# Kernel tuning notes

Hardware: AMD Instinct MI355X
Metric: run time of the kernel (lower is better)

The kernel has to match this reference:

```python
import jax, jax.numpy as jnp
import numpy as np

BATCH = 1024
M = 64      # N_v measurements
N = 8192    # N_theta unknowns
STEPS = 3   # N_admm_steps
EPS_DIV = 1e-12


def setup_inputs() -> dict:
    key = jax.random.key(0)
    k = jax.random.split(key, 4)
    return {
        "r_n": jax.random.normal(k[0], (BATCH, 2, N), jnp.float32),
        "y": jax.random.normal(k[1], (BATCH, 2, M), jnp.float32),
        "u_in": jax.random.normal(k[2], (BATCH, 2, M), jnp.float32),
        "A": jax.random.normal(k[3], (2, M, N), jnp.float32) / np.sqrt(N).astype(np.float32),
        "log_rho": jnp.zeros((), jnp.float32),                 # rho = 1.0
        "log_epsilon": jnp.asarray(np.log(0.01), jnp.float32), # epsilon = 0.01
    }


def _cmm(Ar, Ai, v):
    # complex matmul A @ v : v [b,2,N] -> [b,2,M]
    vr, vi = v[:, 0], v[:, 1]
    return jnp.stack([vr @ Ar.T - vi @ Ai.T, vi @ Ar.T + vr @ Ai.T], axis=1)


def _chm(Ar, Ai, v):
    # complex conj-transpose matmul A^H @ v : v [b,2,M] -> [b,2,N]
    vr, vi = v[:, 0], v[:, 1]
    return jnp.stack([vr @ Ar + vi @ Ai, vi @ Ar - vr @ Ai], axis=1)


def reference(r_n, y, u_in, A, log_rho, log_epsilon):
    rho = jnp.exp(log_rho)
    epsilon = jnp.exp(log_epsilon)
    Ar, Ai = A[0], A[1]  # [M, N]

    # SMW system matrix: S = (1/rho) I + A A^H, written as real 2Mx2M block matrix.
    # It is constant across ADMM steps (rho fixed within a forward pass).
    I_M = jnp.eye(M, dtype=A.dtype)
    S_r = I_M / (rho + EPS_DIV) + Ar @ Ar.T + Ai @ Ai.T
    S_i = Ai @ Ar.T - Ar @ Ai.T
    S_block = jnp.block([[S_r, -S_i], [S_i, S_r]])  # [2M, 2M]

    x, z, u = r_n, y, u_in
    for _ in range(STEPS):
        # x-update via SMW: x = b - A^H (S^{-1} A b), b = r_n + rho A^H (z - u)
        b = r_n + rho * _chm(Ar, Ai, z - u)          # [b,2,N]
        Ab = _cmm(Ar, Ai, b)                          # [b,2,M]
        R = jnp.concatenate([Ab[:, 0], Ab[:, 1]], axis=1)  # [b,2M]
        sol = jnp.linalg.solve(S_block, R.T)          # [2M, b]
        T = jnp.stack([sol[:M].T, sol[M:].T], axis=1)  # [b,2,M]
        x = b - _chm(Ar, Ai, T)                       # [b,2,N]
        # enforce_real: zero imaginary part; enforce_positivity: clamp real part
        x = jnp.stack([jnp.maximum(x[:, 0], 0.0), jnp.zeros_like(x[:, 0])], axis=1)
        # z-update: project residual onto complex L2 ball of radius epsilon
        Ax = _cmm(Ar, Ai, x)                          # [b,2,M]
        v = Ax + u - y
        nrm = jnp.sqrt(jnp.sum(v * v, axis=(1, 2), keepdims=True))
        z = y + v * jnp.minimum(1.0, epsilon / (nrm + EPS_DIV))
        # dual update
        u = u + Ax - z
    return x, u
```

## Files before the change

kernel.cpp:

```cpp
#include <hip/hip_runtime.h>

#define B_ 1024
#define M_ 64
#define N_ 8192
#define NSG 16
#define NS3 8

typedef __attribute__((ext_vector_type(8))) short bf16x8;
typedef __attribute__((ext_vector_type(4))) float f32x4;

__device__ inline unsigned short f2b(float f) {
    union { float f; unsigned u; } v; v.f = f;
    unsigned r = v.u + 0x7FFFu + ((v.u >> 16) & 1u);
    return (unsigned short)(r >> 16);
}
__device__ inline unsigned rne2(float lo, float hi) {
    union { float f; unsigned u; } a, b; a.f = lo; b.f = hi;
    unsigned x = (a.u + 0x7FFFu + ((a.u >> 16) & 1u)) >> 16;
    unsigned y = (b.u + 0x7FFFu + ((b.u >> 16) & 1u)) >> 16;
    return x | (y << 16);
}
__device__ inline float b2f(unsigned short s) {
    union { unsigned u; float f; } v; v.u = ((unsigned)s) << 16; return v.f;
}
__device__ inline float rl(float v, int l) {
    return __builtin_bit_cast(float, __builtin_amdgcn_readlane(__builtin_bit_cast(int, v), l));
}

__global__ __launch_bounds__(256) void k_cvt(const float* src, unsigned short* dst) {
    size_t i = ((size_t)blockIdx.x * 256 + threadIdx.x) * 8;
    float4 f0 = *(const float4*)(src + i);
    float4 f1 = *(const float4*)(src + i + 4);
    union { bf16x8 v; unsigned u[4]; } r;
    r.u[0] = rne2(f0.x, f0.y); r.u[1] = rne2(f0.z, f0.w);
    r.u[2] = rne2(f1.x, f1.y); r.u[3] = rne2(f1.z, f1.w);
    *(bf16x8*)(dst + i) = r.v;
}

__global__ __launch_bounds__(256) void k_prep(const float* A, unsigned short* Abf,
                                              unsigned short* WgT, unsigned short* ATb,
                                              float* out) {
    if (blockIdx.x >= 128) {
        int z = blockIdx.x - 128;
        int fi = z * 4096 + threadIdx.x * 16;
        int b = fi >> 13;
        int n = fi & 8191;
        float4* p = (float4*)(out + (size_t)b * 16384 + 8192 + n);
        float4 z4 = make_float4(0.f, 0.f, 0.f, 0.f);
        p[0] = z4; p[1] = z4; p[2] = z4; p[3] = z4;
        return;
    }
    __shared__ float tile[128][65];
    int n0 = blockIdx.x * 64;
    int t = threadIdx.x;
    int nl = t % 64, r0 = t / 64;
#pragma unroll
    for (int it = 0; it < 32; ++it) {
        int row = r0 + it * 4;
        tile[row][nl] = A[(size_t)row * N_ + n0 + nl];
    }
    __syncthreads();
#pragma unroll
    for (int it = 0; it < 32; ++it) {
        int row = r0 + it * 4;
        float v = tile[row][nl];
        unsigned short bv = f2b(v);
        Abf[(size_t)row * N_ + n0 + nl] = bv;
        if (row < 64) {
            WgT[(size_t)row * 16384 + n0 + nl] = bv;
            WgT[(size_t)(64 + row) * 16384 + 8192 + n0 + nl] = bv;
        } else {
            int m = row - 64;
            WgT[(size_t)m * 16384 + 8192 + n0 + nl] = f2b(-v);
            WgT[(size_t)(64 + m) * 16384 + n0 + nl] = bv;
        }
    }
    int o = t % 128, nn0 = t / 128;
#pragma unroll
    for (int it = 0; it < 32; ++it) {
        int nn = nn0 + it * 2;
        ATb[(size_t)(n0 + nn) * 128 + o] = f2b(tile[o][nn]);
    }
}

__global__ __launch_bounds__(256) void k_Sbuild(const float* A, const float* lr,
                                                float* S, float* AAHT) {
    __shared__ float redS[8];
    int bid = blockIdx.x;
    int i = 0, rem = bid;
    while (rem >= 64 - i) { rem -= 64 - i; ++i; }
    int j = i + rem;
    int t = threadIdx.x;
    const float* Ar = A;
    const float* Ai = A + (size_t)M_ * N_;
    const float* ari = Ar + (size_t)i * N_;
    const float* aii = Ai + (size_t)i * N_;
    const float* arj = Ar + (size_t)j * N_;
    const float* aij = Ai + (size_t)j * N_;
    float aR = 0.f, aI = 0.f;
#pragma unroll
    for (int it = 0; it < 8; ++it) {
        int n = it * 1024 + t * 4;
        float4 xr = *(const float4*)(ari + n);
        float4 xi = *(const float4*)(aii + n);
        float4 br = *(const float4*)(arj + n);
        float4 bi = *(const float4*)(aij + n);
        aR += xr.x * br.x + xi.x * bi.x + xr.y * br.y + xi.y * bi.y
            + xr.z * br.z + xi.z * bi.z + xr.w * br.w + xi.w * bi.w;
        aI += xi.x * br.x - xr.x * bi.x + xi.y * br.y - xr.y * bi.y
            + xi.z * br.z - xr.z * bi.z + xi.w * br.w - xr.w * bi.w;
    }
    for (int off = 32; off > 0; off >>= 1) {
        aR += __shfl_down(aR, off, 64);
        aI += __shfl_down(aI, off, 64);
    }
    int lane = t & 63, w = t >> 6;
    if (lane == 0) { redS[w * 2] = aR; redS[w * 2 + 1] = aI; }
    __syncthreads();
    if (t == 0) {
        float R = redS[0] + redS[2] + redS[4] + redS[6];
        float I = redS[1] + redS[3] + redS[5] + redS[7];
        float inv_rho = 1.0f / (expf(lr[0]) + 1e-12f);
        float diag = (i == j) ? inv_rho : 0.f;
        S[((size_t)i * 64 + j) * 2 + 0] = R + diag;
        S[((size_t)i * 64 + j) * 2 + 1] = I;
        AAHT[((size_t)j * 64 + i) * 2 + 0] = R;
        AAHT[((size_t)j * 64 + i) * 2 + 1] = I;
        if (i != j) {
            S[((size_t)j * 64 + i) * 2 + 0] = R;
            S[((size_t)j * 64 + i) * 2 + 1] = -I;
            AAHT[((size_t)i * 64 + j) * 2 + 0] = R;
            AAHT[((size_t)i * 64 + j) * 2 + 1] = -I;
        }
    }
}

__global__ __launch_bounds__(256, 2) void k_Ginv(const unsigned short* rnb,
                                                 const unsigned short* WgT,
                                                 float* Gpart,
                                                 const float* S, float* Wt) {
    int t = threadIdx.x;
    int lane = t & 63;
    if (blockIdx.x == 0) {
        __builtin_amdgcn_s_setprio(1);
        __shared__ float2 Tp[2][4][64];
        int g = t >> 6;
        float mx0,my0,mx1,my1,mx2,my2,mx3,my3,mx4,my4,mx5,my5,mx6,my6,mx7,my7;
        float mx8,my8,mx9,my9,mx10,my10,mx11,my11,mx12,my12,mx13,my13,mx14,my14,mx15,my15;
#define GJ_INIT(J) { int c = 16 * ((J) >> 2) + 4 * g + ((J) & 3);            \
    float2 v = ((const float2*)S)[(size_t)lane * 64 + c];                    \
    mx##J = v.x; my##J = v.y; }
        GJ_INIT(0) GJ_INIT(1) GJ_INIT(2) GJ_INIT(3) GJ_INIT(4) GJ_INIT(5) GJ_INIT(6) GJ_INIT(7)
        GJ_INIT(8) GJ_INIT(9) GJ_INIT(10) GJ_INIT(11) GJ_INIT(12) GJ_INIT(13) GJ_INIT(14) GJ_INIT(15)
#undef GJ_INIT

#define PIV(JA, JB0, JB1, JB2, jj) {                                         \
    int k = p4 + (jj);                                                       \
    float px = rl(mx##JA, k), py = rl(my##JA, k);                            \
    float d = px * px + py * py;                                             \
    float id = 1.0f / d;                                                     \
    float pix = px * id, piy = -py * id;                                     \
    bool isk = (lane == k);                                                  \
    float a   = isk ? 0.f : 1.f;                                             \
    float fpx = isk ? -pix : (mx##JA * pix - my##JA * piy);                  \
    float fpy = isk ? -piy : (mx##JA * piy + my##JA * pix);                  \
    { float sx = rl(mx##JB0, k), sy = rl(my##JB0, k);                        \
      float nx = a * mx##JB0 - (fpx * sx - fpy * sy);                        \
      float ny = a * my##JB0 - (fpx * sy + fpy * sx);                        \
      mx##JB0 = nx; my##JB0 = ny; }                                          \
    { float sx = rl(mx##JB1, k), sy = rl(my##JB1, k);                        \
      float nx = a * mx##JB1 - (fpx * sx - fpy * sy);                        \
      float ny = a * my##JB1 - (fpx * sy + fpy * sx);                        \
      mx##JB1 = nx; my##JB1 = ny; }                                          \
    { float sx = rl(mx##JB2, k), sy = rl(my##JB2, k);                        \
      float nx = a * mx##JB2 - (fpx * sx - fpy * sy);                        \
      float ny = a * my##JB2 - (fpx * sy + fpy * sx);                        \
      mx##JB2 = nx; my##JB2 = ny; }                                          \
    mx##JA = -fpx; my##JA = -fpy; }

#define FACT4(J0, J1, J2, J3) {                                              \
    PIV(J0, J1, J2, J3, 0) PIV(J1, J0, J2, J3, 1)                            \
    PIV(J2, J0, J1, J3, 2) PIV(J3, J0, J1, J2, 3)                            \
    Tp[buf][0][lane] = make_float2(mx##J0, my##J0);                          \
    Tp[buf][1][lane] = make_float2(mx##J1, my##J1);                          \
    Tp[buf][2][lane] = make_float2(mx##J2, my##J2);                          \
    Tp[buf][3][lane] = make_float2(mx##J3, my##J3); }

        for (int p = 0; p < 16; ++p) {
            const int buf = p & 1;
            const int p4  = p * 4;
            const int q   = p >> 2;
            const bool own = (g == (p & 3));
            if (own) {
                switch (q) {
                    case 0:  FACT4(0, 1, 2, 3)     break;
                    case 1:  FACT4(4, 5, 6, 7)     break;
                    case 2:  FACT4(8, 9, 10, 11)   break;
                    default: FACT4(12, 13, 14, 15) break;
                }
            }
            __syncthreads();
            float2 t0 = Tp[buf][0][lane];
            float2 t1 = Tp[buf][1][lane];
            float2 t2 = Tp[buf][2][lane];
            float2 t3 = Tp[buf][3][lane];
            float msk = ((lane >> 2) == p) ? 0.f : 1.f;
            int skipq = own ? q : -1;
#define TRAIL(J) if (((J) >> 2) != skipq) {                                  \
    float s0x = rl(mx##J, p4),     s0y = rl(my##J, p4);                      \
    float s1x = rl(mx##J, p4 + 1), s1y = rl(my##J, p4 + 1);                  \
    float s2x = rl(mx##J, p4 + 2), s2y = rl(my##J, p4 + 2);                  \
    float s3x = rl(mx##J, p4 + 3), s3y = rl(my##J, p4 + 3);                  \
    float ax = msk * mx##J, ay = msk * my##J;                                \
    ax += t0.x * s0x - t0.y * s0y; ay += t0.x * s0y + t0.y * s0x;            \
    ax += t1.x * s1x - t1.y * s1y; ay += t1.x * s1y + t1.y * s1x;            \
    ax += t2.x * s2x - t2.y * s2y; ay += t2.x * s2y + t2.y * s2x;            \
    ax += t3.x * s3x - t3.y * s3y; ay += t3.x * s3y + t3.y * s3x;            \
    mx##J = ax; my##J = ay; }
            TRAIL(0)  TRAIL(1)  TRAIL(2)  TRAIL(3)
            TRAIL(4)  TRAIL(5)  TRAIL(6)  TRAIL(7)
            TRAIL(8)  TRAIL(9)  TRAIL(10) TRAIL(11)
            TRAIL(12) TRAIL(13) TRAIL(14) TRAIL(15)
#undef TRAIL
        }
#undef FACT4
#undef PIV
#define GJ_OUT(J) { int c = 16 * ((J) >> 2) + 4 * g + ((J) & 3);             \
    ((float2*)Wt)[(size_t)c * 64 + lane] = make_float2(mx##J, my##J); }
        GJ_OUT(0) GJ_OUT(1) GJ_OUT(2) GJ_OUT(3) GJ_OUT(4) GJ_OUT(5) GJ_OUT(6) GJ_OUT(7)
        GJ_OUT(8) GJ_OUT(9) GJ_OUT(10) GJ_OUT(11) GJ_OUT(12) GJ_OUT(13) GJ_OUT(14) GJ_OUT(15)
#undef GJ_OUT
        __builtin_amdgcn_s_setprio(0);
    }
    int bx = blockIdx.x;
    int w = t >> 6;
    int l15 = lane & 15;
    int q8 = (lane >> 4) * 8;
    int split = bx & 15;
    int b0 = (bx >> 4) * 32;
    int k0 = split * 1024;
    f32x4 a00 = {}, a01 = {}, a10 = {}, a11 = {};
    const unsigned short* x0 = rnb + (size_t)(b0 + l15) * 16384 + k0 + q8;
    const unsigned short* x1 = x0 + (size_t)16 * 16384;
    const unsigned short* w0 = WgT + (size_t)(w * 32 + l15) * 16384 + k0 + q8;
    const unsigned short* w1 = w0 + (size_t)16 * 16384;
#pragma unroll 8
    for (int ks = 0; ks < 32; ++ks) {
        int kk = ks * 32;
        bf16x8 af0 = *(const bf16x8*)(x0 + kk);
        bf16x8 af1 = *(const bf16x8*)(x1 + kk);
        bf16x8 bf0 = *(const bf16x8*)(w0 + kk);
        bf16x8 bf1 = *(const bf16x8*)(w1 + kk);
        a00 = __builtin_amdgcn_mfma_f32_16x16x32_bf16(af0, bf0, a00, 0, 0, 0);
        a01 = __builtin_amdgcn_mfma_f32_16x16x32_bf16(af0, bf1, a01, 0, 0, 0);
        a10 = __builtin_amdgcn_mfma_f32_16x16x32_bf16(af1, bf0, a10, 0, 0, 0);
        a11 = __builtin_amdgcn_mfma_f32_16x16x32_bf16(af1, bf1, a11, 0, 0, 0);
    }
    int row = (lane >> 4) * 4;
    size_t base = (size_t)split * (B_ * 128);
    float* g  = Gpart + base + (size_t)(b0 + row) * 128 + w * 32 + l15;
    float* g2 = g + 16 * 128;
#pragma unroll
    for (int r = 0; r < 4; ++r) {
        g[(size_t)r * 128]       = a00[r];
        g[(size_t)r * 128 + 16]  = a01[r];
        g2[(size_t)r * 128]      = a10[r];
        g2[(size_t)r * 128 + 16] = a11[r];
    }
}

__global__ __launch_bounds__(256) void k_F(const float* Gpart, const float* AAHT,
                                           const float* Wt, const float* Axpart,
                                           const float* y, const float* uprev,
                                           float* u, const float* lr, const float* le,
                                           unsigned short* qb, int have_ax) {
    __shared__ float wS[128];
    __shared__ float2 partA[4][64];
    __shared__ float2 partB[4][64];
    __shared__ float2 AbS[64];
    __shared__ float red[2];
    int t = threadIdx.x;
    int b = blockIdx.x;
    float rho = expf(lr[0]);
    if (have_ax) {
        float vv = 0.f, uo = 0.f, yv = 0.f, ax = 0.f;
        if (t < 128) {
            size_t idx = (size_t)b * 128 + t;
            #pragma unroll
            for (int s = 0; s < NS3; ++s) ax += Axpart[(size_t)s * 131072 + idx];
            uo = uprev[idx]; yv = y[idx];
            vv = ax + uo - yv;
            float sq = vv * vv;
            for (int off = 32; off > 0; off >>= 1) sq += __shfl_down(sq, off, 64);
            if ((t & 63) == 0) red[t >> 6] = sq;
        }
        __syncthreads();
        if (t < 128) {
            float tot = red[0] + red[1];
            float eps = expf(le[0]);
            float scale = fminf(1.f, eps / (sqrtf(tot) + 1e-12f));
            float zv = yv + vv * scale;
            float un = uo + ax - zv;
            u[(size_t)b * 128 + t] = un;
            wS[t] = zv - un;
        }
    } else {
        if (t < 128) {
            size_t idx = (size_t)b * 128 + t;
            wS[t] = y[idx] - uprev[idx];
        }
    }
    __syncthreads();
    int m = t & 63;
    int w = __builtin_amdgcn_readfirstlane(t >> 6);
    float aR = 0.f, aI = 0.f;
#pragma unroll
    for (int kk = 0; kk < 16; ++kk) {
        int k = w * 16 + kk;
        float wr = wS[k];
        float wi = wS[64 + k];
        float2 h = *(const float2*)(AAHT + ((size_t)k * 64 + m) * 2);
        aR += wr * h.x - wi * h.y;
        aI += wi * h.x + wr * h.y;
    }
    aR *= rho; aI *= rho;
#pragma unroll
    for (int s4 = 0; s4 < 4; ++s4) {
        int s = w * 4 + s4;
        aR += Gpart[(size_t)s * 131072 + (size_t)b * 128 + m];
        aI += Gpart[(size_t)s * 131072 + (size_t)b * 128 + 64 + m];
    }
    partA[w][m] = make_float2(aR, aI);
    __syncthreads();
    if (w == 0) {
        float2 p0 = partA[0][m], p1 = partA[1][m], p2 = partA[2][m], p3 = partA[3][m];
        AbS[m] = make_float2(p0.x + p1.x + p2.x + p3.x, p0.y + p1.y + p2.y + p3.y);
    }
    __syncthreads();
    float tR = 0.f, tI = 0.f;
#pragma unroll
    for (int kk = 0; kk < 16; ++kk) {
        int k = w * 16 + kk;
        float2 Wv = *(const float2*)(Wt + ((size_t)k * 64 + m) * 2);
        float2 ab = AbS[k];
        tR += ab.x * Wv.x - ab.y * Wv.y;
        tI += ab.y * Wv.x + ab.x * Wv.y;
    }
    partB[w][m] = make_float2(tR, tI);
    __syncthreads();
    if (w == 0) {
        float2 q0 = partB[0][m], q1 = partB[1][m], q2 = partB[2][m], q3 = partB[3][m];
        float sR = q0.x + q1.x + q2.x + q3.x;
        float sI = q0.y + q1.y + q2.y + q3.y;
        qb[(size_t)b * 128 + m] = f2b(rho * wS[m] - sR);
        qb[(size_t)b * 128 + 64 + m] = f2b(rho * wS[64 + m] - sI);
    }
}

__global__ __launch_bounds__(512, 2) void k_H23(const unsigned short* qb, const unsigned short* ATb,
                                                const unsigned short* rnb, const unsigned short* Abf,
                                                float* out, float* Axpart, int last) {
    __shared__ __align__(16) char lds_buf[8 * 8448];
    int t = threadIdx.x;
    int lane = t & 63;
    int w = t >> 6;
    int l15 = lane & 15;
    int q8 = (lane >> 4) * 8;
    int row = (lane >> 4) * 4;
    int slab = blockIdx.x;
    int b0 = blockIdx.y * 16;
    int n0 = slab * 1024 + w * 128;
    short* xs = (short*)(lds_buf + w * 8448);
    float* rs = (float*)(lds_buf + w * 8448);

    bf16x8 a[4];
    const unsigned short* qrow = qb + (size_t)(b0 + l15) * 128 + q8;
#pragma unroll
    for (int ks = 0; ks < 4; ++ks) a[ks] = *(const bf16x8*)(qrow + ks * 32);
#pragma unroll 2
    for (int nt = 0; nt < 8; ++nt) {
        f32x4 acc = {};
        const unsigned short* bbase = ATb + (size_t)(n0 + nt * 16 + l15) * 128 + q8;
#pragma unroll
        for (int ks = 0; ks < 4; ++ks) {
            bf16x8 bf = *(const bf16x8*)(bbase + ks * 32);
            acc = __builtin_amdgcn_mfma_f32_16x16x32_bf16(a[ks], bf, acc, 0, 0, 0);
        }
        int ncol = n0 + nt * 16 + l15;
        int nloc = nt * 16 + l15;
#pragma unroll
        for (int r = 0; r < 4; ++r) {
            size_t ridx = (size_t)(b0 + row + r) * 16384 + ncol;
            float v = fmaxf(acc[r] + b2f(rnb[ridx]), 0.f);
            if (last) out[ridx] = v;
            xs[(row + r) * 264 + nloc] = (short)f2b(v);
        }
    }
    f32x4 acc8[8] = {};
#pragma unroll
    for (int ks = 0; ks < 4; ++ks) {
        bf16x8 xf = *(const bf16x8*)(xs + l15 * 264 + ks * 32 + q8);
#pragma unroll
        for (int ot = 0; ot < 8; ++ot) {
            const unsigned short* bp = Abf + (size_t)(ot * 16 + l15) * 8192 + n0 + ks * 32 + q8;
            acc8[ot] = __builtin_amdgcn_mfma_f32_16x16x32_bf16(xf, *(const bf16x8*)bp, acc8[ot], 0, 0, 0);
        }
    }
    __syncthreads();
#pragma unroll
    for (int ot = 0; ot < 8; ++ot)
#pragma unroll
        for (int r = 0; r < 4; ++r)
            rs[(row + r) * 132 + ot * 16 + l15] = acc8[ot][r];
    __syncthreads();
#pragma unroll
    for (int e = t; e < 2048; e += 512) {
        int b = e >> 7, o = e & 127;
        float sAx = 0.f;
#pragma unroll
        for (int ww = 0; ww < 8; ++ww)
            sAx += ((const float*)(lds_buf + ww * 8448))[b * 132 + o];
        Axpart[(size_t)slab * 131072 + (size_t)(b0 + b) * 128 + o] = sAx;
    }
}

__global__ __launch_bounds__(128) void k_small3f(const float* Axpart, const float* uprev,
                                                 const float* y, const float* le,
                                                 float* uout) {
    __shared__ float red[2];
    int b = blockIdx.x, t = threadIdx.x;
    size_t idx = (size_t)b * 128 + t;
    float ax = 0.f;
#pragma unroll
    for (int s = 0; s < NS3; ++s) ax += Axpart[(size_t)s * 131072 + idx];
    float uo = uprev[idx], yv = y[idx];
    float v = ax + uo - yv;
    float sq = v * v;
    for (int off = 32; off > 0; off >>= 1) sq += __shfl_down(sq, off, 64);
    if ((t & 63) == 0) red[t >> 6] = sq;
    __syncthreads();
    float tot = red[0] + red[1];
    float eps = expf(le[0]);
    float scale = fminf(1.f, eps / (sqrtf(tot) + 1e-12f));
    float zv = yv + v * scale;
    float un = uo + ax - zv;
    uout[idx] = un;
}

extern "C" void kernel_launch(void* const* d_in, const int* in_sizes, int n_in,
                              void* d_out, int out_size, void* d_ws, size_t ws_size,
                              hipStream_t stream) {
    const float* rn  = (const float*)d_in[0];
    const float* y   = (const float*)d_in[1];
    const float* uin = (const float*)d_in[2];
    const float* A   = (const float*)d_in[3];
    const float* lr  = (const float*)d_in[4];
    const float* le  = (const float*)d_in[5];

    float* out = (float*)d_out;
    float* ws  = (float*)d_ws;

    float* Gpart  = ws;
    float* Axpart = Gpart + (size_t)NSG * 131072;
    float* S      = Axpart + (size_t)NS3 * 131072;
    float* AAHT   = S + 8192;
    float* Wt     = AAHT + 8192;
    float* z      = Wt + 8192;
    float* u      = z + 131072;
    unsigned short* qb  = (unsigned short*)(u + 131072);
    unsigned short* rnb = qb + 131072;
    unsigned short* WgT = rnb + (size_t)B_ * 16384;
    unsigned short* Abf = WgT + 2097152;
    unsigned short* ATb = Abf + 1048576;
    float* uout = out + (size_t)B_ * 2 * N_;

    k_prep<<<2176, 256, 0, stream>>>(A, Abf, WgT, ATb, out);
    k_cvt<<<8192, 256, 0, stream>>>(rn, rnb);
    k_Sbuild<<<2080, 256, 0, stream>>>(A, lr, S, AAHT);
    k_Ginv<<<512, 256, 0, stream>>>(rnb, WgT, Gpart, S, Wt);

    k_F<<<B_, 256, 0, stream>>>(Gpart, AAHT, Wt, Axpart, y, uin, u, lr, le, qb, 0);
    k_H23<<<dim3(NS3, 64), 512, 0, stream>>>(qb, ATb, rnb, Abf, out, Axpart, 0);
    k_F<<<B_, 256, 0, stream>>>(Gpart, AAHT, Wt, Axpart, y, uin, u, lr, le, qb, 1);
    k_H23<<<dim3(NS3, 64), 512, 0, stream>>>(qb, ATb, rnb, Abf, out, Axpart, 0);
    k_F<<<B_, 256, 0, stream>>>(Gpart, AAHT, Wt, Axpart, y, u, u, lr, le, qb, 1);
    k_H23<<<dim3(NS3, 64), 512, 0, stream>>>(qb, ATb, rnb, Abf, out, Axpart, 1);
    k_small3f<<<B_, 128, 0, stream>>>(Axpart, u, y, le, uout);
}
```

Measured before the change: 337.9 us.

## Split Gauss-Jordan into own kernel, halve H23 slab width, broadcast pivot rows via LDS

Moves the 64x64 complex Gauss-Jordan inversion out of block 0 of k_Ginv into a separate single-block kernel. It also replaces the per-column readlane pivot-row broadcasts with an LDS staging buffer (Srow). k_H23 now covers 512 columns per slab across 16 slabs instead of 1024 across 8, which shrinks LDS use and adds a two-phase in-LDS reduction of the per-wave partial results. The intent is more parallelism and occupancy in the x/Ax kernel and shorter serial chains in GJ. In exchange, k_small3f reads more Axpart partials, the GJ step becomes a serial one-block launch, and an unused z buffer is dropped from the workspace.

```diff
diff --git a/kernel.cpp b/kernel.cpp
--- a/kernel.cpp
+++ b/kernel.cpp
@@ -4,7 +4,7 @@
 #define M_ 64
 #define N_ 8192
 #define NSG 16
-#define NS3 8
+#define NS3 16
 
 typedef __attribute__((ext_vector_type(8))) short bf16x8;
 typedef __attribute__((ext_vector_type(4))) float f32x4;
@@ -135,23 +135,19 @@
     }
 }
 
-__global__ __launch_bounds__(256, 2) void k_Ginv(const unsigned short* rnb,
-                                                 const unsigned short* WgT,
-                                                 float* Gpart,
-                                                 const float* S, float* Wt) {
+__global__ __launch_bounds__(256) void k_gj(const float* S, float* Wt) {
     int t = threadIdx.x;
     int lane = t & 63;
-    if (blockIdx.x == 0) {
-        __builtin_amdgcn_s_setprio(1);
-        __shared__ float2 Tp[2][4][64];
-        int g = t >> 6;
-        float mx0,my0,mx1,my1,mx2,my2,mx3,my3,mx4,my4,mx5,my5,mx6,my6,mx7,my7;
-        float mx8,my8,mx9,my9,mx10,my10,mx11,my11,mx12,my12,mx13,my13,mx14,my14,mx15,my15;
+    int g = t >> 6;
+    __shared__ float2 Tp[2][4][64];
+    __shared__ float2 Srow[4][4][16];
+    float mx0,my0,mx1,my1,mx2,my2,mx3,my3,mx4,my4,mx5,my5,mx6,my6,mx7,my7;
+    float mx8,my8,mx9,my9,mx10,my10,mx11,my11,mx12,my12,mx13,my13,mx14,my14,mx15,my15;
 #define GJ_INIT(J) { int c = 16 * ((J) >> 2) + 4 * g + ((J) & 3);            \
     float2 v = ((const float2*)S)[(size_t)lane * 64 + c];                    \
     mx##J = v.x; my##J = v.y; }
-        GJ_INIT(0) GJ_INIT(1) GJ_INIT(2) GJ_INIT(3) GJ_INIT(4) GJ_INIT(5) GJ_INIT(6) GJ_INIT(7)
-        GJ_INIT(8) GJ_INIT(9) GJ_INIT(10) GJ_INIT(11) GJ_INIT(12) GJ_INIT(13) GJ_INIT(14) GJ_INIT(15)
+    GJ_INIT(0) GJ_INIT(1) GJ_INIT(2) GJ_INIT(3) GJ_INIT(4) GJ_INIT(5) GJ_INIT(6) GJ_INIT(7)
+    GJ_INIT(8) GJ_INIT(9) GJ_INIT(10) GJ_INIT(11) GJ_INIT(12) GJ_INIT(13) GJ_INIT(14) GJ_INIT(15)
 #undef GJ_INIT
 
 #define PIV(JA, JB0, JB1, JB2, jj) {                                         \
@@ -186,52 +182,74 @@
     Tp[buf][2][lane] = make_float2(mx##J2, my##J2);                          \
     Tp[buf][3][lane] = make_float2(mx##J3, my##J3); }
 
-        for (int p = 0; p < 16; ++p) {
-            const int buf = p & 1;
-            const int p4  = p * 4;
-            const int q   = p >> 2;
-            const bool own = (g == (p & 3));
-            if (own) {
-                switch (q) {
-                    case 0:  FACT4(0, 1, 2, 3)     break;
-                    case 1:  FACT4(4, 5, 6, 7)     break;
-                    case 2:  FACT4(8, 9, 10, 11)   break;
-                    default: FACT4(12, 13, 14, 15) break;
-                }
+    for (int p = 0; p < 16; ++p) {
+        const int buf = p & 1;
+        const int p4  = p * 4;
+        const int q   = p >> 2;
+        const bool own = (g == (p & 3));
+        if ((lane >> 2) == p) {
+            int j = lane & 3;
+            Srow[g][j][0]  = make_float2(mx0,  my0);
+            Srow[g][j][1]  = make_float2(mx1,  my1);
+            Srow[g][j][2]  = make_float2(mx2,  my2);
+            Srow[g][j][3]  = make_float2(mx3,  my3);
+            Srow[g][j][4]  = make_float2(mx4,  my4);
+            Srow[g][j][5]  = make_float2(mx5,  my5);
+            Srow[g][j][6]  = make_float2(mx6,  my6);
+            Srow[g][j][7]  = make_float2(mx7,  my7);
+            Srow[g][j][8]  = make_float2(mx8,  my8);
+            Srow[g][j][9]  = make_float2(mx9,  my9);
+            Srow[g][j][10] = make_float2(mx10, my10);
+            Srow[g][j][11] = make_float2(mx11, my11);
+            Srow[g][j][12] = make_float2(mx12, my12);
+            Srow[g][j][13] = make_float2(mx13, my13);
+            Srow[g][j][14] = make_float2(mx14, my14);
+            Srow[g][j][15] = make_float2(mx15, my15);
+        }
+        if (own) {
+            switch (q) {
+                case 0:  FACT4(0, 1, 2, 3)     break;
+                case 1:  FACT4(4, 5, 6, 7)     break;
+                case 2:  FACT4(8, 9, 10, 11)   break;
+                default: FACT4(12, 13, 14, 15) break;
             }
-            __syncthreads();
-            float2 t0 = Tp[buf][0][lane];
-            float2 t1 = Tp[buf][1][lane];
-            float2 t2 = Tp[buf][2][lane];
-            float2 t3 = Tp[buf][3][lane];
-            float msk = ((lane >> 2) == p) ? 0.f : 1.f;
-            int skipq = own ? q : -1;
+        }
+        __syncthreads();
+        float2 t0 = Tp[buf][0][lane];
+        float2 t1 = Tp[buf][1][lane];
+        float2 t2 = Tp[buf][2][lane];
+        float2 t3 = Tp[buf][3][lane];
+        float msk = ((lane >> 2) == p) ? 0.f : 1.f;
+        int skipq = own ? q : -1;
 #define TRAIL(J) if (((J) >> 2) != skipq) {                                  \
-    float s0x = rl(mx##J, p4),     s0y = rl(my##J, p4);                      \
-    float s1x = rl(mx##J, p4 + 1), s1y = rl(my##J, p4 + 1);                  \
-    float s2x = rl(mx##J, p4 + 2), s2y = rl(my##J, p4 + 2);                  \
-    float s3x = rl(mx##J, p4 + 3), s3y = rl(my##J, p4 + 3);                  \
+    float2 s0 = Srow[g][0][J], s1 = Srow[g][1][J];                           \
+    float2 s2 = Srow[g][2][J], s3 = Srow[g][3][J];                           \
     float ax = msk * mx##J, ay = msk * my##J;                                \
-    ax += t0.x * s0x - t0.y * s0y; ay += t0.x * s0y + t0.y * s0x;            \
-    ax += t1.x * s1x - t1.y * s1y; ay += t1.x * s1y + t1.y * s1x;            \
-    ax += t2.x * s2x - t2.y * s2y; ay += t2.x * s2y + t2.y * s2x;            \
-    ax += t3.x * s3x - t3.y * s3y; ay += t3.x * s3y + t3.y * s3x;            \
+    ax += t0.x * s0.x - t0.y * s0.y; ay += t0.x * s0.y + t0.y * s0.x;        \
+    ax += t1.x * s1.x - t1.y * s1.y; ay += t1.x * s1.y + t1.y * s1.x;        \
+    ax += t2.x * s2.x - t2.y * s2.y; ay += t2.x * s2.y + t2.y * s2.x;        \
+    ax += t3.x * s3.x - t3.y * s3.y; ay += t3.x * s3.y + t3.y * s3.x;        \
     mx##J = ax; my##J = ay; }
-            TRAIL(0)  TRAIL(1)  TRAIL(2)  TRAIL(3)
-            TRAIL(4)  TRAIL(5)  TRAIL(6)  TRAIL(7)
-            TRAIL(8)  TRAIL(9)  TRAIL(10) TRAIL(11)
-            TRAIL(12) TRAIL(13) TRAIL(14) TRAIL(15)
+        TRAIL(0)  TRAIL(1)  TRAIL(2)  TRAIL(3)
+        TRAIL(4)  TRAIL(5)  TRAIL(6)  TRAIL(7)
+        TRAIL(8)  TRAIL(9)  TRAIL(10) TRAIL(11)
+        TRAIL(12) TRAIL(13) TRAIL(14) TRAIL(15)
 #undef TRAIL
-        }
+    }
 #undef FACT4
 #undef PIV
 #define GJ_OUT(J) { int c = 16 * ((J) >> 2) + 4 * g + ((J) & 3);             \
     ((float2*)Wt)[(size_t)c * 64 + lane] = make_float2(mx##J, my##J); }
-        GJ_OUT(0) GJ_OUT(1) GJ_OUT(2) GJ_OUT(3) GJ_OUT(4) GJ_OUT(5) GJ_OUT(6) GJ_OUT(7)
-        GJ_OUT(8) GJ_OUT(9) GJ_OUT(10) GJ_OUT(11) GJ_OUT(12) GJ_OUT(13) GJ_OUT(14) GJ_OUT(15)
+    GJ_OUT(0) GJ_OUT(1) GJ_OUT(2) GJ_OUT(3) GJ_OUT(4) GJ_OUT(5) GJ_OUT(6) GJ_OUT(7)
+    GJ_OUT(8) GJ_OUT(9) GJ_OUT(10) GJ_OUT(11) GJ_OUT(12) GJ_OUT(13) GJ_OUT(14) GJ_OUT(15)
 #undef GJ_OUT
-        __builtin_amdgcn_s_setprio(0);
-    }
+}
+
+__global__ __launch_bounds__(256, 2) void k_Ginv(const unsigned short* rnb,
+                                                 const unsigned short* WgT,
+                                                 float* Gpart) {
+    int t = threadIdx.x;
+    int lane = t & 63;
     int bx = blockIdx.x;
     int w = t >> 6;
     int l15 = lane & 15;
@@ -360,7 +378,7 @@
 __global__ __launch_bounds__(512, 2) void k_H23(const unsigned short* qb, const unsigned short* ATb,
                                                 const unsigned short* rnb, const unsigned short* Abf,
                                                 float* out, float* Axpart, int last) {
-    __shared__ __align__(16) char lds_buf[8 * 8448];
+    __shared__ __align__(16) char lds_buf[33792];
     int t = threadIdx.x;
     int lane = t & 63;
     int w = t >> 6;
@@ -369,16 +387,15 @@
     int row = (lane >> 4) * 4;
     int slab = blockIdx.x;
     int b0 = blockIdx.y * 16;
-    int n0 = slab * 1024 + w * 128;
-    short* xs = (short*)(lds_buf + w * 8448);
-    float* rs = (float*)(lds_buf + w * 8448);
+    int n0 = slab * 512 + w * 64;
+    short* xs = (short*)(lds_buf + w * 2304);
 
     bf16x8 a[4];
     const unsigned short* qrow = qb + (size_t)(b0 + l15) * 128 + q8;
 #pragma unroll
     for (int ks = 0; ks < 4; ++ks) a[ks] = *(const bf16x8*)(qrow + ks * 32);
-#pragma unroll 2
-    for (int nt = 0; nt < 8; ++nt) {
+#pragma unroll
+    for (int nt = 0; nt < 4; ++nt) {
         f32x4 acc = {};
         const unsigned short* bbase = ATb + (size_t)(n0 + nt * 16 + l15) * 128 + q8;
 #pragma unroll
@@ -393,13 +410,13 @@
             size_t ridx = (size_t)(b0 + row + r) * 16384 + ncol;
             float v = fmaxf(acc[r] + b2f(rnb[ridx]), 0.f);
             if (last) out[ridx] = v;
-            xs[(row + r) * 264 + nloc] = (short)f2b(v);
+            xs[(row + r) * 72 + nloc] = (short)f2b(v);
         }
     }
     f32x4 acc8[8] = {};
 #pragma unroll
-    for (int ks = 0; ks < 4; ++ks) {
-        bf16x8 xf = *(const bf16x8*)(xs + l15 * 264 + ks * 32 + q8);
+    for (int ks = 0; ks < 2; ++ks) {
+        bf16x8 xf = *(const bf16x8*)(xs + l15 * 72 + ks * 32 + q8);
 #pragma unroll
         for (int ot = 0; ot < 8; ++ot) {
             const unsigned short* bp = Abf + (size_t)(ot * 16 + l15) * 8192 + n0 + ks * 32 + q8;
@@ -407,19 +424,30 @@
         }
     }
     __syncthreads();
-#pragma unroll
-    for (int ot = 0; ot < 8; ++ot)
-#pragma unroll
-        for (int r = 0; r < 4; ++r)
-            rs[(row + r) * 132 + ot * 16 + l15] = acc8[ot][r];
+    float* slot = (float*)(lds_buf + (w & 3) * 8448);
+    if (w >= 4) {
+#pragma unroll
+        for (int ot = 0; ot < 8; ++ot)
+#pragma unroll
+            for (int r = 0; r < 4; ++r)
+                slot[(row + r) * 132 + ot * 16 + l15] = acc8[ot][r];
+    }
+    __syncthreads();
+    if (w < 4) {
+#pragma unroll
+        for (int ot = 0; ot < 8; ++ot)
+#pragma unroll
+            for (int r = 0; r < 4; ++r)
+                slot[(row + r) * 132 + ot * 16 + l15] += acc8[ot][r];
+    }
     __syncthreads();
 #pragma unroll
     for (int e = t; e < 2048; e += 512) {
         int b = e >> 7, o = e & 127;
         float sAx = 0.f;
 #pragma unroll
-        for (int ww = 0; ww < 8; ++ww)
-            sAx += ((const float*)(lds_buf + ww * 8448))[b * 132 + o];
+        for (int s4 = 0; s4 < 4; ++s4)
+            sAx += ((const float*)(lds_buf + s4 * 8448))[b * 132 + o];
         Axpart[(size_t)slab * 131072 + (size_t)(b0 + b) * 128 + o] = sAx;
     }
 }
@@ -465,8 +493,7 @@
     float* S      = Axpart + (size_t)NS3 * 131072;
     float* AAHT   = S + 8192;
     float* Wt     = AAHT + 8192;
-    float* z      = Wt + 8192;
-    float* u      = z + 131072;
+    float* u      = Wt + 8192;
     unsigned short* qb  = (unsigned short*)(u + 131072);
     unsigned short* rnb = qb + 131072;
     unsigned short* WgT = rnb + (size_t)B_ * 16384;
@@ -477,7 +504,8 @@
     k_prep<<<2176, 256, 0, stream>>>(A, Abf, WgT, ATb, out);
     k_cvt<<<8192, 256, 0, stream>>>(rn, rnb);
     k_Sbuild<<<2080, 256, 0, stream>>>(A, lr, S, AAHT);
-    k_Ginv<<<512, 256, 0, stream>>>(rnb, WgT, Gpart, S, Wt);
+    k_gj<<<1, 256, 0, stream>>>(S, Wt);
+    k_Ginv<<<512, 256, 0, stream>>>(rnb, WgT, Gpart);
 
     k_F<<<B_, 256, 0, stream>>>(Gpart, AAHT, Wt, Axpart, y, uin, u, lr, le, qb, 0);
     k_H23<<<dim3(NS3, 64), 512, 0, stream>>>(qb, ATb, rnb, Abf, out, Axpart, 0);
```

Result: slower. 360.2 us (+6.6%).
